# Optimization experiments

Measured on AMD Instinct MI355X. Metric: run time of the kernel, lower is better.

The kernel has to match this reference:

```python
import jax, jax.numpy as jnp
import numpy as np

N, L, H = 64, 1024, 1024

def setup_inputs() -> dict:
    key = jax.random.key(0)
    ks = jax.random.split(key, 6)
    scale = 1.0 / np.sqrt(H)
    return {
        "decoder_hidden": jax.random.normal(ks[0], (N, H), dtype=jnp.float32),
        "encoder_hiddens": jax.random.normal(ks[1], (N, L, H), dtype=jnp.float32),
        "mask": jax.random.randint(ks[2], (N, L), 0, 2) > 0,  # True = PAD position
        "W_h": jax.random.normal(ks[3], (H, H), dtype=jnp.float32) * scale,
        "W_s": jax.random.normal(ks[4], (H, H), dtype=jnp.float32) * scale,
        "v": jax.random.normal(ks[5], (H,), dtype=jnp.float32) * scale,
    }

def reference(decoder_hidden, encoder_hiddens, mask, W_h, W_s, v):
    # score(h_t, h_s) = v^T tanh(W_h h_t + W_s h_s)
    # torch Linear: y = x @ W.T
    dh = decoder_hidden @ W_h.T                      # [N, H]
    eh = jnp.einsum('nlh,kh->nlk', encoder_hiddens, W_s)  # [N, L, H]
    score = jnp.tanh(dh[:, None, :] + eh) @ v        # [N, L]
    score = jnp.where(mask, -jnp.inf, score)
    attn_weights = jax.nn.softmax(score, axis=1)     # [N, L]
    context = jnp.einsum('nl,nlh->nh', attn_weights, encoder_hiddens)  # [N, H]
    return (context, attn_weights)
```

## Files before the change

kernel.cpp:

```cpp
#include <hip/hip_runtime.h>
#include <hip/hip_bf16.h>
#include <math.h>

#define N_  64
#define L_  1024
#define H_  1024
#define NL_ (N_ * L_)

typedef __attribute__((ext_vector_type(8))) short bf16x8;
typedef __attribute__((ext_vector_type(4))) float f32x4;
typedef unsigned short ushort_t;
typedef unsigned int uint_t;

__device__ inline ushort_t f32_to_bf16_rne(float f) {
    uint_t u = __float_as_uint(f);
    u += 0x7FFFu + ((u >> 16) & 1u);
    return (ushort_t)(u >> 16);
}

__global__ __launch_bounds__(256) void convert_bf16_kernel(const float* __restrict__ src,
                                                           ushort_t* __restrict__ dst) {
    size_t i = ((size_t)blockIdx.x * 256 + threadIdx.x) * 8;
    float4 a = *(const float4*)(src + i);
    float4 b = *(const float4*)(src + i + 4);
    union { bf16x8 v; ushort_t u[8]; } o;
    o.u[0] = f32_to_bf16_rne(a.x); o.u[1] = f32_to_bf16_rne(a.y);
    o.u[2] = f32_to_bf16_rne(a.z); o.u[3] = f32_to_bf16_rne(a.w);
    o.u[4] = f32_to_bf16_rne(b.x); o.u[5] = f32_to_bf16_rne(b.y);
    o.u[6] = f32_to_bf16_rne(b.z); o.u[7] = f32_to_bf16_rne(b.w);
    *(bf16x8*)(dst + i) = o.v;
}

__global__ __launch_bounds__(256) void dh_kernel(const float* __restrict__ ddec,
                                                 const float* __restrict__ Wh,
                                                 float* __restrict__ dh) {
    int i = blockIdx.x * 256 + threadIdx.x;
    int n = i >> 10;
    const float* a = ddec + (size_t)n * H_;
    const float* w = Wh + (size_t)(i & (H_ - 1)) * H_;
    float acc = 0.f;
#pragma unroll 4
    for (int h = 0; h < H_; h += 4) {
        float4 av = *(const float4*)(a + h);
        float4 wv = *(const float4*)(w + h);
        acc += av.x * wv.x + av.y * wv.y + av.z * wv.z + av.w * wv.w;
    }
    dh[i] = acc;
}

__device__ inline void stage_tile(const ushort_t* __restrict__ gbase,
                                  ushort_t* lds, int tid, size_t row0_off) {
#pragma unroll
    for (int j = 0; j < 2; j++) {
        int c_lin = j * 256 + tid;
        int r  = c_lin >> 2;
        int cp = c_lin & 3;
        int q  = cp ^ ((r >> 1) & 3);
        const ushort_t* g = gbase + row0_off + (size_t)r * H_ + q * 8;
        ushort_t* l = lds + (size_t)(j * 256 + (tid & ~63)) * 8;
        __builtin_amdgcn_global_load_lds((const __attribute__((address_space(1))) void*)g,
                                         (__attribute__((address_space(3))) void*)l,
                                         16, 0, 0);
    }
}

__global__ __launch_bounds__(256) void score_mfma_kernel(const ushort_t* __restrict__ enc_bf,
                                                         const ushort_t* __restrict__ ws_bf,
                                                         const float* __restrict__ dh,
                                                         const float* __restrict__ v,
                                                         float* __restrict__ score) {
    __shared__ ushort_t As[128 * 32];
    __shared__ ushort_t Bs[128 * 32];

    const int i0 = blockIdx.x * 128;
    const int k0 = blockIdx.y * 128;
    const int tid  = threadIdx.x;
    const int lane = tid & 63;
    const int wv   = tid >> 6;
    const int wr   = (wv >> 1) * 64;
    const int wc   = (wv & 1) * 64;
    const int m    = lane & 15;
    const int q    = lane >> 4;
    const int qs   = q ^ ((m >> 1) & 3);

    f32x4 acc[4][4];
#pragma unroll
    for (int a = 0; a < 4; a++)
#pragma unroll
        for (int b = 0; b < 4; b++)
            acc[a][b] = (f32x4){0.f, 0.f, 0.f, 0.f};

    for (int h0 = 0; h0 < H_; h0 += 32) {
        __syncthreads();
        stage_tile(enc_bf, As, tid, (size_t)i0 * H_ + h0);
        stage_tile(ws_bf,  Bs, tid, (size_t)k0 * H_ + h0);
        __syncthreads();

        bf16x8 af[4], bfr[4];
#pragma unroll
        for (int ti = 0; ti < 4; ti++) {
            int r = wr + ti * 16 + m;
            af[ti] = *(const bf16x8*)(As + (size_t)(r * 4 + qs) * 8);
        }
#pragma unroll
        for (int tj = 0; tj < 4; tj++) {
            int r = wc + tj * 16 + m;
            bfr[tj] = *(const bf16x8*)(Bs + (size_t)(r * 4 + qs) * 8);
        }
#pragma unroll
        for (int ti = 0; ti < 4; ti++)
#pragma unroll
            for (int tj = 0; tj < 4; tj++)
                acc[ti][tj] = __builtin_amdgcn_mfma_f32_16x16x32_bf16(
                    af[ti], bfr[tj], acc[ti][tj], 0, 0, 0);
    }

    const int nb = i0 >> 10;
    float vv[4], dhv[4];
#pragma unroll
    for (int tj = 0; tj < 4; tj++) {
        int k = k0 + wc + tj * 16 + m;
        vv[tj]  = v[k];
        dhv[tj] = dh[nb * H_ + k];
    }
#pragma unroll
    for (int ti = 0; ti < 4; ti++) {
#pragma unroll
        for (int reg = 0; reg < 4; reg++) {
            float s = 0.f;
#pragma unroll
            for (int tj = 0; tj < 4; tj++) {
                float x  = dhv[tj] + acc[ti][tj][reg];
                float e2 = __expf(2.f * x);
                s += vv[tj] * (1.f - 2.f / (e2 + 1.f));
            }
            s += __shfl_xor(s, 1);
            s += __shfl_xor(s, 2);
            s += __shfl_xor(s, 4);
            s += __shfl_xor(s, 8);
            if (m == 0) {
                int i_local = wr + ti * 16 + q * 4 + reg;
                atomicAdd(&score[i0 + i_local], s);
            }
        }
    }
}

__global__ __launch_bounds__(256) void softmax_kernel(const float* __restrict__ score,
                                                      const int* __restrict__ mask,
                                                      float* __restrict__ attn) {
    const int n = blockIdx.x;
    const int t = threadIdx.x;
    __shared__ float redmax[4];
    __shared__ float redsum[4];

    float s[4];
    int   mk[4];
    float mymax = -INFINITY;
#pragma unroll
    for (int j = 0; j < 4; j++) {
        int l = t + j * 256;
        mk[j] = mask[n * L_ + l];
        s[j] = mk[j] ? -INFINITY : score[n * L_ + l];
        mymax = fmaxf(mymax, s[j]);
    }
#pragma unroll
    for (int off = 1; off < 64; off <<= 1)
        mymax = fmaxf(mymax, __shfl_xor(mymax, off));
    if ((t & 63) == 0) redmax[t >> 6] = mymax;
    __syncthreads();
    float gmax = fmaxf(fmaxf(redmax[0], redmax[1]), fmaxf(redmax[2], redmax[3]));

    float e[4];
    float mysum = 0.f;
#pragma unroll
    for (int j = 0; j < 4; j++) {
        e[j] = mk[j] ? 0.f : __expf(s[j] - gmax);
        mysum += e[j];
    }
#pragma unroll
    for (int off = 1; off < 64; off <<= 1)
        mysum += __shfl_xor(mysum, off);
    if ((t & 63) == 0) redsum[t >> 6] = mysum;
    __syncthreads();
    float gsum = redsum[0] + redsum[1] + redsum[2] + redsum[3];
    float inv = 1.f / gsum;
#pragma unroll
    for (int j = 0; j < 4; j++)
        attn[n * L_ + t + j * 256] = e[j] * inv;
}

__global__ __launch_bounds__(256) void context_kernel(const ushort_t* __restrict__ enc_bf,
                                                      const float* __restrict__ attn,
                                                      float* __restrict__ ctx) {
    const int n = blockIdx.x;
    const int h = blockIdx.y * 256 + threadIdx.x;
    __shared__ float w[L_];
#pragma unroll
    for (int j = 0; j < 4; j++)
        w[threadIdx.x + j * 256] = attn[n * L_ + threadIdx.x + j * 256];
    __syncthreads();

    const ushort_t* e = enc_bf + (size_t)n * L_ * H_ + h;
    float acc = 0.f;
#pragma unroll 8
    for (int l = 0; l < L_; l++) {
        float x = __uint_as_float(((uint_t)e[(size_t)l * H_]) << 16);
        acc += w[l] * x;
    }
    ctx[n * H_ + h] = acc;
}

extern "C" void kernel_launch(void* const* d_in, const int* in_sizes, int n_in,
                              void* d_out, int out_size, void* d_ws, size_t ws_size,
                              hipStream_t stream) {
    const float* ddec = (const float*)d_in[0];
    const float* enc  = (const float*)d_in[1];
    const int*   mask = (const int*)d_in[2];
    const float* Wh   = (const float*)d_in[3];
    const float* Ws   = (const float*)d_in[4];
    const float* v    = (const float*)d_in[5];

    float* out_ctx  = (float*)d_out;
    float* out_attn = out_ctx + N_ * H_;

    ushort_t* enc_bf = (ushort_t*)d_ws;
    ushort_t* ws_bf  = enc_bf + (size_t)NL_ * H_;
    float*    dh     = (float*)(ws_bf + (size_t)H_ * H_);
    float*    score  = dh + N_ * H_;

    convert_bf16_kernel<<<(size_t)NL_ * H_ / 2048, 256, 0, stream>>>(enc, enc_bf);
    convert_bf16_kernel<<<(size_t)H_ * H_ / 2048, 256, 0, stream>>>(Ws, ws_bf);

    hipMemsetAsync(score, 0, (size_t)NL_ * sizeof(float), stream);

    dh_kernel<<<NL_ / 256, 256, 0, stream>>>(ddec, Wh, dh);

    dim3 g2(NL_ / 128, H_ / 128);
    score_mfma_kernel<<<g2, 256, 0, stream>>>(enc_bf, ws_bf, dh, v, score);

    softmax_kernel<<<N_, 256, 0, stream>>>(score, mask, out_attn);

    dim3 g4(N_, 4);
    context_kernel<<<g4, 256, 0, stream>>>(enc_bf, out_attn, out_ctx);
}
```

Before: 677.0 us.

## Split context over L with atomics, swizzle score block order, grid-stride convert

The context kernel now splits the sequence dimension into 8 chunks per batch, reads 8 bf16 values per thread as a vector, and accumulates partial sums into a zeroed output with atomics. This replaces the old 256-block launch with a strided scalar 2-byte read per thread. The score GEMM uses a 1D grid remapped so groups of 8 row tiles by 8 column tiles run together, aiming for better L2 reuse of encoder and weight tiles. The bf16 conversion becomes a grid-stride loop with a fixed grid, and the dh loop unroll is raised, at the cost of an extra memset and atomic contention.

```diff
diff --git a/kernel.cpp b/kernel.cpp
--- a/kernel.cpp
+++ b/kernel.cpp
@@ -19,16 +19,20 @@
 }
 
 __global__ __launch_bounds__(256) void convert_bf16_kernel(const float* __restrict__ src,
-                                                           ushort_t* __restrict__ dst) {
-    size_t i = ((size_t)blockIdx.x * 256 + threadIdx.x) * 8;
-    float4 a = *(const float4*)(src + i);
-    float4 b = *(const float4*)(src + i + 4);
-    union { bf16x8 v; ushort_t u[8]; } o;
-    o.u[0] = f32_to_bf16_rne(a.x); o.u[1] = f32_to_bf16_rne(a.y);
-    o.u[2] = f32_to_bf16_rne(a.z); o.u[3] = f32_to_bf16_rne(a.w);
-    o.u[4] = f32_to_bf16_rne(b.x); o.u[5] = f32_to_bf16_rne(b.y);
-    o.u[6] = f32_to_bf16_rne(b.z); o.u[7] = f32_to_bf16_rne(b.w);
-    *(bf16x8*)(dst + i) = o.v;
+                                                           ushort_t* __restrict__ dst,
+                                                           size_t nvec8) {
+    size_t stride = (size_t)gridDim.x * 256;
+    for (size_t g = (size_t)blockIdx.x * 256 + threadIdx.x; g < nvec8; g += stride) {
+        size_t i = g * 8;
+        float4 a = *(const float4*)(src + i);
+        float4 b = *(const float4*)(src + i + 4);
+        union { bf16x8 v; ushort_t u[8]; } o;
+        o.u[0] = f32_to_bf16_rne(a.x); o.u[1] = f32_to_bf16_rne(a.y);
+        o.u[2] = f32_to_bf16_rne(a.z); o.u[3] = f32_to_bf16_rne(a.w);
+        o.u[4] = f32_to_bf16_rne(b.x); o.u[5] = f32_to_bf16_rne(b.y);
+        o.u[6] = f32_to_bf16_rne(b.z); o.u[7] = f32_to_bf16_rne(b.w);
+        *(bf16x8*)(dst + i) = o.v;
+    }
 }
 
 __global__ __launch_bounds__(256) void dh_kernel(const float* __restrict__ ddec,
@@ -39,7 +43,7 @@
     const float* a = ddec + (size_t)n * H_;
     const float* w = Wh + (size_t)(i & (H_ - 1)) * H_;
     float acc = 0.f;
-#pragma unroll 4
+#pragma unroll 8
     for (int h = 0; h < H_; h += 4) {
         float4 av = *(const float4*)(a + h);
         float4 wv = *(const float4*)(w + h);
@@ -72,8 +76,9 @@
     __shared__ ushort_t As[128 * 32];
     __shared__ ushort_t Bs[128 * 32];
 
-    const int i0 = blockIdx.x * 128;
-    const int k0 = blockIdx.y * 128;
+    const int b  = blockIdx.x;
+    const int i0 = ((b & 7) | ((b >> 6) << 3)) * 128;
+    const int k0 = ((b >> 3) & 7) * 128;
     const int tid  = threadIdx.x;
     const int lane = tid & 63;
     const int wv   = tid >> 6;
@@ -87,8 +92,8 @@
 #pragma unroll
     for (int a = 0; a < 4; a++)
 #pragma unroll
-        for (int b = 0; b < 4; b++)
-            acc[a][b] = (f32x4){0.f, 0.f, 0.f, 0.f};
+        for (int c = 0; c < 4; c++)
+            acc[a][c] = (f32x4){0.f, 0.f, 0.f, 0.f};
 
     for (int h0 = 0; h0 < H_; h0 += 32) {
         __syncthreads();
@@ -190,25 +195,32 @@
         attn[n * L_ + t + j * 256] = e[j] * inv;
 }
 
-__global__ __launch_bounds__(256) void context_kernel(const ushort_t* __restrict__ enc_bf,
+__global__ __launch_bounds__(128) void context_kernel(const ushort_t* __restrict__ enc_bf,
                                                       const float* __restrict__ attn,
                                                       float* __restrict__ ctx) {
-    const int n = blockIdx.x;
-    const int h = blockIdx.y * 256 + threadIdx.x;
-    __shared__ float w[L_];
-#pragma unroll
-    for (int j = 0; j < 4; j++)
-        w[threadIdx.x + j * 256] = attn[n * L_ + threadIdx.x + j * 256];
+    const int n  = blockIdx.x;
+    const int l0 = blockIdx.y * 128;
+    const int t  = threadIdx.x;
+    const int h0 = t * 8;
+
+    __shared__ float w[128];
+    w[t] = attn[n * L_ + l0 + t];
     __syncthreads();
 
-    const ushort_t* e = enc_bf + (size_t)n * L_ * H_ + h;
-    float acc = 0.f;
-#pragma unroll 8
-    for (int l = 0; l < L_; l++) {
-        float x = __uint_as_float(((uint_t)e[(size_t)l * H_]) << 16);
-        acc += w[l] * x;
-    }
-    ctx[n * H_ + h] = acc;
+    const ushort_t* base = enc_bf + (size_t)n * L_ * H_ + (size_t)l0 * H_ + h0;
+    float acc[8] = {};
+#pragma unroll 4
+    for (int l = 0; l < 128; l++) {
+        union { bf16x8 v; ushort_t u[8]; } e;
+        e.v = *(const bf16x8*)(base + (size_t)l * H_);
+        float wl = w[l];
+#pragma unroll
+        for (int j = 0; j < 8; j++)
+            acc[j] += wl * __uint_as_float(((uint_t)e.u[j]) << 16);
+    }
+#pragma unroll
+    for (int j = 0; j < 8; j++)
+        atomicAdd(&ctx[n * H_ + h0 + j], acc[j]);
 }
 
 extern "C" void kernel_launch(void* const* d_in, const int* in_sizes, int n_in,
@@ -229,18 +241,18 @@
     float*    dh     = (float*)(ws_bf + (size_t)H_ * H_);
     float*    score  = dh + N_ * H_;
 
-    convert_bf16_kernel<<<(size_t)NL_ * H_ / 2048, 256, 0, stream>>>(enc, enc_bf);
-    convert_bf16_kernel<<<(size_t)H_ * H_ / 2048, 256, 0, stream>>>(Ws, ws_bf);
+    convert_bf16_kernel<<<4096, 256, 0, stream>>>(enc, enc_bf, (size_t)NL_ * H_ / 8);
+    convert_bf16_kernel<<<512, 256, 0, stream>>>(Ws, ws_bf, (size_t)H_ * H_ / 8);
 
     hipMemsetAsync(score, 0, (size_t)NL_ * sizeof(float), stream);
+    hipMemsetAsync(out_ctx, 0, (size_t)N_ * H_ * sizeof(float), stream);
 
     dh_kernel<<<NL_ / 256, 256, 0, stream>>>(ddec, Wh, dh);
 
-    dim3 g2(NL_ / 128, H_ / 128);
-    score_mfma_kernel<<<g2, 256, 0, stream>>>(enc_bf, ws_bf, dh, v, score);
+    score_mfma_kernel<<<4096, 256, 0, stream>>>(enc_bf, ws_bf, dh, v, score);
 
     softmax_kernel<<<N_, 256, 0, stream>>>(score, mask, out_attn);
 
-    dim3 g4(N_, 4);
-    context_kernel<<<g4, 256, 0, stream>>>(enc_bf, out_attn, out_ctx);
-}
+    dim3 g4(N_, 8);
+    context_kernel<<<g4, 128, 0, stream>>>(enc_bf, out_attn, out_ctx);
+}
```

New measurement: 659.7 us. 1.03x faster.
